# Optimization experiments

Hardware: AMD Instinct MI355X
Metric: run time of the kernel (lower is better)

The kernel has to match this reference:

```python
import jax, jax.numpy as jnp
import numpy as np
from math import sqrt

INPUT, HIDDEN, OUTPUT = 256, 512, 256
B, T = 64, 1024


def setup_inputs() -> dict:
    key = jax.random.key(0)
    k1, k2, k3, k4 = jax.random.split(key, 4)
    x = jax.random.normal(k1, (B, T, INPUT), dtype=jnp.float32)
    W_xh = jax.random.normal(k2, (INPUT, HIDDEN), dtype=jnp.float32) * sqrt(2.0 / (INPUT + HIDDEN))
    W_hh = jax.random.normal(k3, (HIDDEN, HIDDEN), dtype=jnp.float32) * sqrt(1.0 / HIDDEN)
    b_h = jnp.zeros((HIDDEN,), dtype=jnp.float32)
    W_hy = jax.random.normal(k4, (HIDDEN, OUTPUT), dtype=jnp.float32) * sqrt(2.0 / (HIDDEN + OUTPUT))
    b_y = jnp.zeros((OUTPUT,), dtype=jnp.float32)
    return {"x": x, "W_xh": W_xh, "W_hh": W_hh, "b_h": b_h, "W_hy": W_hy, "b_y": b_y}


def reference(x, W_xh, W_hh, b_h, W_hy, b_y):
    # Precompute input projection for all timesteps: [B,T,H_in] @ [H_in,H] -> [B,T,H]
    xh = jnp.einsum('bti,ih->bth', x, W_xh) + b_h
    h0 = jnp.zeros((x.shape[0], W_hh.shape[0]), dtype=x.dtype)

    def step(h, xh_t):
        h_new = jnp.tanh(h @ W_hh + xh_t)  # [B,H]
        return h_new, h_new

    # scan over time: xh transposed to [T,B,H]
    _, hs = jax.lax.scan(step, h0, jnp.swapaxes(xh, 0, 1))
    hs = jnp.swapaxes(hs, 0, 1)  # [B,T,H]
    outputs = jnp.einsum('bth,ho->bto', hs, W_hy) + b_y  # [B,T,O]
    return outputs
```

## Files before the change

### kernel.cpp

```cpp
#include <hip/hip_runtime.h>
#include <hip/hip_bf16.h>
#include <hip/hip_fp16.h>


#define BT 65536
#define HID 512
#define NIN 256
#define NOUT 256
#define TSTEPS 1024
#define NBATCH 64

typedef _Float16 hf2_t __attribute__((ext_vector_type(2)));

__device__ __forceinline__ float fdot2(unsigned w, unsigned h, float acc) {
#if __has_builtin(__builtin_amdgcn_fdot2)
    return __builtin_amdgcn_fdot2(__builtin_bit_cast(hf2_t, w),
                                  __builtin_bit_cast(hf2_t, h), acc, false);
#else
    __half2 wv = __builtin_bit_cast(__half2, w);
    __half2 hv = __builtin_bit_cast(__half2, h);
    float2 wf = __half22float2(wv);
    float2 hf = __half22float2(hv);
    return acc + wf.x * hf.x + wf.y * hf.y;
#endif
}

__device__ __forceinline__ float dot4(uint4 w, uint4 h, float acc) {
    acc = fdot2(w.x, h.x, acc);
    acc = fdot2(w.y, h.y, acc);
    acc = fdot2(w.z, h.z, acc);
    acc = fdot2(w.w, h.w, acc);
    return acc;
}

__device__ __forceinline__ unsigned pack2h(float a, float b) {
    unsigned lo = (unsigned)__half_as_ushort(__float2half_rn(a));
    unsigned hi = (unsigned)__half_as_ushort(__float2half_rn(b));
    return lo | (hi << 16);
}

template <int CTRL>
__device__ __forceinline__ float dpp_add(float x) {
    int y = __builtin_amdgcn_mov_dpp(__float_as_int(x), CTRL, 0xF, 0xF, true);
    return x + __int_as_float(y);
}

__device__ __forceinline__ float fast_tanh(float x) {
    float e = __builtin_amdgcn_exp2f(x * 2.8853900817779268f);
    return 1.0f - 2.0f * __builtin_amdgcn_rcpf(e + 1.0f);
}

__device__ __forceinline__ float4 load4f(const float* p) {
    return *(const float4*)p;
}
__device__ __forceinline__ float4 load4f(const __half* p) {
    ushort4 u = *(const ushort4*)p;
    float4 r;
    r.x = __half2float(__ushort_as_half(u.x));
    r.y = __half2float(__ushort_as_half(u.y));
    r.z = __half2float(__ushort_as_half(u.z));
    r.w = __half2float(__ushort_as_half(u.w));
    return r;
}
__device__ __forceinline__ void store1(float* p, float v) { *p = v; }
__device__ __forceinline__ void store1(__half* p, float v) { *p = __float2half_rn(v); }

__global__ __launch_bounds__(256)
void pack_w_kernel(const float* __restrict__ W,
                   unsigned* __restrict__ reg_blob,
                   unsigned* __restrict__ gcol_blob) {
    int t = blockIdx.x;
    int w = threadIdx.x;
    int q = t >> 2, s = t & 3, k0 = 128 * s;
    if (w < 192) {
        int c = w >> 6, m = w & 63;
        int col = 4 * q + c, k = k0 + 2 * m;
        unsigned val = pack2h(W[(size_t)k * HID + col], W[(size_t)(k + 1) * HID + col]);
        int i = w >> 2, u = w & 3;
        reg_blob[i * 2048 + t * 4 + u] = val;
    } else {
        int m = w - 192;
        int col = 4 * q + 3, k = k0 + 2 * m;
        unsigned val = pack2h(W[(size_t)k * HID + col], W[(size_t)(k + 1) * HID + col]);
        int j = m >> 2, u = m & 3;
        gcol_blob[j * 2048 + t * 4 + u] = val;
    }
}

template <typename AT, typename CT>
__global__ __launch_bounds__(256)
void gemm_bias_kernel(const AT* __restrict__ A, const float* __restrict__ B,
                      const float* __restrict__ bias, CT* __restrict__ C,
                      int M, int N, int K) {
    const int TM = 64, TN = 64, TK = 16;
    __shared__ float As[TK][TM];
    __shared__ float Bs[TK][TN + 4];

    int tid = threadIdx.x;
    int tx = tid & 15;
    int ty = tid >> 4;
    int row0 = blockIdx.x * TM;
    int col0 = blockIdx.y * TN;

    float c[4][4];
#pragma unroll
    for (int i = 0; i < 4; ++i)
#pragma unroll
        for (int j = 0; j < 4; ++j) c[i][j] = 0.f;

    for (int kk = 0; kk < K; kk += TK) {
        {
            int ar = tid >> 2;
            int ac = (tid & 3) * 4;
            float4 av = load4f(A + (size_t)(row0 + ar) * K + kk + ac);
            As[ac + 0][ar] = av.x;
            As[ac + 1][ar] = av.y;
            As[ac + 2][ar] = av.z;
            As[ac + 3][ar] = av.w;
        }
        {
            int br = tid >> 4;
            int bc = (tid & 15) * 4;
            float4 bv = *(const float4*)(B + (size_t)(kk + br) * N + col0 + bc);
            *(float4*)&Bs[br][bc] = bv;
        }
        __syncthreads();
#pragma unroll
        for (int k = 0; k < TK; ++k) {
            float4 a = *(const float4*)&As[k][ty * 4];
            float4 b = *(const float4*)&Bs[k][tx * 4];
            float av[4] = {a.x, a.y, a.z, a.w};
            float bv[4] = {b.x, b.y, b.z, b.w};
#pragma unroll
            for (int i = 0; i < 4; ++i)
#pragma unroll
                for (int j = 0; j < 4; ++j) c[i][j] += av[i] * bv[j];
        }
        __syncthreads();
    }

#pragma unroll
    for (int j = 0; j < 4; ++j) {
        float bb = bias[col0 + tx * 4 + j];
#pragma unroll
        for (int i = 0; i < 4; ++i) {
            int r = row0 + ty * 4 + i;
            int cc = col0 + tx * 4 + j;
            store1(&C[(size_t)r * N + cc], c[i][j] + bb);
        }
    }
}

template <typename AT, typename CT>
__global__ __launch_bounds__(256)
void gemm_bias_f16_kernel(const AT* __restrict__ A, const float* __restrict__ B,
                          const float* __restrict__ bias, CT* __restrict__ C,
                          int M, int N, int K) {
    const int TM = 64, TN = 64, TK = 16;
    __shared__ unsigned Asp[TK / 2][TM];
    __shared__ unsigned Bsp[TK / 2][TN + 4];

    int tid = threadIdx.x;
    int tx = tid & 15;
    int ty = tid >> 4;
    int row0 = blockIdx.x * TM;
    int col0 = blockIdx.y * TN;

    float c[4][4];
#pragma unroll
    for (int i = 0; i < 4; ++i)
#pragma unroll
        for (int j = 0; j < 4; ++j) c[i][j] = 0.f;

    for (int kk = 0; kk < K; kk += TK) {
        {
            int ar = tid >> 2;
            int ac = (tid & 3) * 4;
            float4 av = load4f(A + (size_t)(row0 + ar) * K + kk + ac);
            Asp[(ac >> 1) + 0][ar] = pack2h(av.x, av.y);
            Asp[(ac >> 1) + 1][ar] = pack2h(av.z, av.w);
        }
        {
            int k2 = tid >> 5;
            int bc = (tid & 31) * 2;
            const float* b0 = B + (size_t)(kk + 2 * k2) * N + col0 + bc;
            const float* b1 = b0 + N;
            float2 r0 = *(const float2*)b0;
            float2 r1 = *(const float2*)b1;
            Bsp[k2][bc + 0] = pack2h(r0.x, r1.x);
            Bsp[k2][bc + 1] = pack2h(r0.y, r1.y);
        }
        __syncthreads();
#pragma unroll
        for (int k2 = 0; k2 < TK / 2; ++k2) {
            uint4 ap = *(const uint4*)&Asp[k2][ty * 4];
            uint4 bp = *(const uint4*)&Bsp[k2][tx * 4];
            unsigned av[4] = {ap.x, ap.y, ap.z, ap.w};
            unsigned bv[4] = {bp.x, bp.y, bp.z, bp.w};
#pragma unroll
            for (int i = 0; i < 4; ++i)
#pragma unroll
                for (int j = 0; j < 4; ++j) c[i][j] = fdot2(av[i], bv[j], c[i][j]);
        }
        __syncthreads();
    }

#pragma unroll
    for (int j = 0; j < 4; ++j) {
        float bb = bias[col0 + tx * 4 + j];
#pragma unroll
        for (int i = 0; i < 4; ++i) {
            int r = row0 + ty * 4 + i;
            int cc = col0 + tx * 4 + j;
            store1(&C[(size_t)r * N + cc], c[i][j] + bb);
        }
    }
}

template <int GLN>
__global__ __launch_bounds__(512, 2)
void rnn_scan_single(const __half* __restrict__ xh,
                     const uint4* __restrict__ reg_blob,
                     const uint4* __restrict__ gcol_blob,
                     __half* __restrict__ hs) {
    __shared__ __align__(16) __half hbuf[2][4][136];
    extern __shared__ __align__(16) uint4 gl_[];

    const int t = threadIdx.x;
    const int b = blockIdx.x;
    const int s = t & 3;

    uint4 W[48];
#pragma unroll
    for (int i = 0; i < 48; ++i) W[i] = reg_blob[i * 512 + t];
#pragma unroll
    for (int j = 0; j < GLN; ++j) gl_[j * 512 + t] = gcol_blob[j * 512 + t];

    hbuf[0][t >> 7][t & 127] = __ushort_as_half((unsigned short)0);
    hbuf[1][t >> 7][t & 127] = __ushort_as_half((unsigned short)0);
    __syncthreads();

    const __half* xp = xh + (size_t)b * TSTEPS * HID + t;
    __half* hp = hs + (size_t)b * TSTEPS * HID + t;
    const uint4* gb = gcol_blob + t;

#define GETG(j) (((j) < GLN) ? gl_[(j) * 512 + t] : gb[(size_t)(j) * 512])

    int cur = 0;
    __half prev = __ushort_as_half((unsigned short)0);

    for (int step = 0; step < TSTEPS; ++step) {
        float xv = __half2float(xp[(size_t)step * HID]);
        if (step) hp[(size_t)(step - 1) * HID] = prev;

        const uint4* hv = (const uint4*)&hbuf[cur][s][0];
        float a0 = 0.f, a1 = 0.f, a2 = 0.f, a3 = 0.f;

#pragma unroll
        for (int ch = 0; ch < 4; ++ch) {
            uint4 g0 = GETG(ch * 4 + 0);
            uint4 g1 = GETG(ch * 4 + 1);
            uint4 g2 = GETG(ch * 4 + 2);
            uint4 g3 = GETG(ch * 4 + 3);
            uint4 h0 = hv[ch * 4 + 0];
            uint4 h1 = hv[ch * 4 + 1];
            uint4 h2 = hv[ch * 4 + 2];
            uint4 h3 = hv[ch * 4 + 3];
            a0 = dot4(W[ch * 4 + 0], h0, a0);
            a1 = dot4(W[16 + ch * 4 + 0], h0, a1);
            a2 = dot4(W[32 + ch * 4 + 0], h0, a2);
            a0 = dot4(W[ch * 4 + 1], h1, a0);
            a1 = dot4(W[16 + ch * 4 + 1], h1, a1);
            a2 = dot4(W[32 + ch * 4 + 1], h1, a2);
            a0 = dot4(W[ch * 4 + 2], h2, a0);
            a1 = dot4(W[16 + ch * 4 + 2], h2, a1);
            a2 = dot4(W[32 + ch * 4 + 2], h2, a2);
            a0 = dot4(W[ch * 4 + 3], h3, a0);
            a1 = dot4(W[16 + ch * 4 + 3], h3, a1);
            a2 = dot4(W[32 + ch * 4 + 3], h3, a2);
            a3 = dot4(g0, h0, a3);
            a3 = dot4(g1, h1, a3);
            a3 = dot4(g2, h2, a3);
            a3 = dot4(g3, h3, a3);
        }
#undef GETG

        a0 = dpp_add<0xB1>(a0); a0 = dpp_add<0x4E>(a0);
        a1 = dpp_add<0xB1>(a1); a1 = dpp_add<0x4E>(a1);
        a2 = dpp_add<0xB1>(a2); a2 = dpp_add<0x4E>(a2);
        a3 = dpp_add<0xB1>(a3); a3 = dpp_add<0x4E>(a3);
        float tot = (s == 0) ? a0 : (s == 1) ? a1 : (s == 2) ? a2 : a3;

        float hn = fast_tanh(tot + xv);
        prev = __float2half_rn(hn);
        hbuf[cur ^ 1][t >> 7][t & 127] = prev;
        __syncthreads();
        cur ^= 1;
    }
    hp[(size_t)(TSTEPS - 1) * HID] = prev;
}

extern "C" void kernel_launch(void* const* d_in, const int* in_sizes, int n_in,
                              void* d_out, int out_size, void* d_ws, size_t ws_size,
                              hipStream_t stream) {
    const float* x    = (const float*)d_in[0];
    const float* W_xh = (const float*)d_in[1];
    const float* W_hh = (const float*)d_in[2];
    const float* b_h  = (const float*)d_in[3];
    const float* W_hy = (const float*)d_in[4];
    const float* b_y  = (const float*)d_in[5];
    float* out = (float*)d_out;

    char* ws = (char*)d_ws;
    const size_t off_gcol = 48 * 512 * 16;
    const size_t off_xh   = (size_t)1 << 20;
    const size_t off_hs   = off_xh + (size_t)BT * HID * 2;

    unsigned* reg_blob  = (unsigned*)ws;
    unsigned* gcol_blob = (unsigned*)(ws + off_gcol);
    __half*   xh        = (__half*)(ws + off_xh);
    __half*   hs        = (__half*)(ws + off_hs);

    pack_w_kernel<<<dim3(512), dim3(256), 0, stream>>>(W_hh, reg_blob, gcol_blob);

    gemm_bias_kernel<float, __half>
        <<<dim3(BT / 64, HID / 64), dim3(256), 0, stream>>>(x, W_xh, b_h, xh, BT, HID, NIN);

    const int GL16_BYTES = 16 * 512 * 16;
    hipError_t e = hipFuncSetAttribute(
        reinterpret_cast<const void*>(&rnn_scan_single<16>),
        hipFuncAttributeMaxDynamicSharedMemorySize, GL16_BYTES);
    if (e == hipSuccess) {
        rnn_scan_single<16><<<dim3(NBATCH), dim3(512), GL16_BYTES, stream>>>(
            xh, (const uint4*)reg_blob, (const uint4*)gcol_blob, hs);
    } else {
        (void)hipGetLastError();
        rnn_scan_single<7><<<dim3(NBATCH), dim3(512), 7 * 512 * 16, stream>>>(
            xh, (const uint4*)reg_blob, (const uint4*)gcol_blob, hs);
    }

    gemm_bias_f16_kernel<__half, float>
        <<<dim3(BT / 64, NOUT / 64), dim3(256), 0, stream>>>(hs, W_hy, b_y, out, BT, NOUT, HID);
}
```

Measured before the change: 1.887 ms.

## Restructure RNN scan to 8-way K split with 8 columns per thread group

Measured after the change: 1.869 ms. Within noise of the previous version (-1.0%).

```diff
diff --git a/kernel.cpp b/kernel.cpp
--- a/kernel.cpp
+++ b/kernel.cpp
@@ -44,6 +44,11 @@
     int y = __builtin_amdgcn_mov_dpp(__float_as_int(x), CTRL, 0xF, 0xF, true);
     return x + __int_as_float(y);
 }
+template <int CTRL>
+__device__ __forceinline__ float dpp_get(float x) {
+    int y = __builtin_amdgcn_mov_dpp(__float_as_int(x), CTRL, 0xF, 0xF, true);
+    return __int_as_float(y);
+}
 
 __device__ __forceinline__ float fast_tanh(float x) {
     float e = __builtin_amdgcn_exp2f(x * 2.8853900817779268f);
@@ -71,20 +76,14 @@
                    unsigned* __restrict__ gcol_blob) {
     int t = blockIdx.x;
     int w = threadIdx.x;
-    int q = t >> 2, s = t & 3, k0 = 128 * s;
-    if (w < 192) {
-        int c = w >> 6, m = w & 63;
-        int col = 4 * q + c, k = k0 + 2 * m;
-        unsigned val = pack2h(W[(size_t)k * HID + col], W[(size_t)(k + 1) * HID + col]);
-        int i = w >> 2, u = w & 3;
-        reg_blob[i * 2048 + t * 4 + u] = val;
-    } else {
-        int m = w - 192;
-        int col = 4 * q + 3, k = k0 + 2 * m;
-        unsigned val = pack2h(W[(size_t)k * HID + col], W[(size_t)(k + 1) * HID + col]);
-        int j = m >> 2, u = m & 3;
-        gcol_blob[j * 2048 + t * 4 + u] = val;
-    }
+    int i = w >> 2, u = w & 3;
+    int g = t >> 3, s = t & 7;
+    int c = i >> 3, j = i & 7;
+    int col = 8 * g + c;
+    int k = 64 * s + 8 * j + 2 * u;
+    unsigned val = pack2h(W[(size_t)k * HID + col], W[(size_t)(k + 1) * HID + col]);
+    if (i < 48) reg_blob[(i * 512 + t) * 4 + u] = val;
+    else        gcol_blob[((i - 48) * 512 + t) * 4 + u] = val;
 }
 
 template <typename AT, typename CT>
@@ -219,16 +218,16 @@
 
 template <int GLN>
 __global__ __launch_bounds__(512, 2)
-void rnn_scan_single(const __half* __restrict__ xh,
-                     const uint4* __restrict__ reg_blob,
-                     const uint4* __restrict__ gcol_blob,
-                     __half* __restrict__ hs) {
-    __shared__ __align__(16) __half hbuf[2][4][136];
+void rnn_scan8(const __half* __restrict__ xh,
+               const uint4* __restrict__ reg_blob,
+               const uint4* __restrict__ gcol_blob,
+               __half* __restrict__ hs) {
+    __shared__ __align__(16) uint4 hbuf4[2][72];
     extern __shared__ __align__(16) uint4 gl_[];
 
     const int t = threadIdx.x;
     const int b = blockIdx.x;
-    const int s = t & 3;
+    const int g = t >> 3, s = t & 7;
 
     uint4 W[48];
 #pragma unroll
@@ -236,13 +235,19 @@
 #pragma unroll
     for (int j = 0; j < GLN; ++j) gl_[j * 512 + t] = gcol_blob[j * 512 + t];
 
-    hbuf[0][t >> 7][t & 127] = __ushort_as_half((unsigned short)0);
-    hbuf[1][t >> 7][t & 127] = __ushort_as_half((unsigned short)0);
+    if (t < 72) {
+        hbuf4[0][t] = uint4{0u, 0u, 0u, 0u};
+        hbuf4[1][t] = uint4{0u, 0u, 0u, 0u};
+    }
     __syncthreads();
 
-    const __half* xp = xh + (size_t)b * TSTEPS * HID + t;
-    __half* hp = hs + (size_t)b * TSTEPS * HID + t;
+    const int col = 8 * g + s;
+    const __half* xp = xh + (size_t)b * TSTEPS * HID + col;
+    __half* hp = hs + (size_t)b * TSTEPS * HID + col;
     const uint4* gb = gcol_blob + t;
+
+    const int H = col >> 1;
+    const int wordC = ((H >> 5) * 9 + ((H >> 2) & 7)) * 4 + (H & 3);
 
 #define GETG(j) (((j) < GLN) ? gl_[(j) * 512 + t] : gb[(size_t)(j) * 512])
 
@@ -253,47 +258,62 @@
         float xv = __half2float(xp[(size_t)step * HID]);
         if (step) hp[(size_t)(step - 1) * HID] = prev;
 
-        const uint4* hv = (const uint4*)&hbuf[cur][s][0];
-        float a0 = 0.f, a1 = 0.f, a2 = 0.f, a3 = 0.f;
-
-#pragma unroll
-        for (int ch = 0; ch < 4; ++ch) {
-            uint4 g0 = GETG(ch * 4 + 0);
-            uint4 g1 = GETG(ch * 4 + 1);
-            uint4 g2 = GETG(ch * 4 + 2);
-            uint4 g3 = GETG(ch * 4 + 3);
-            uint4 h0 = hv[ch * 4 + 0];
-            uint4 h1 = hv[ch * 4 + 1];
-            uint4 h2 = hv[ch * 4 + 2];
-            uint4 h3 = hv[ch * 4 + 3];
-            a0 = dot4(W[ch * 4 + 0], h0, a0);
-            a1 = dot4(W[16 + ch * 4 + 0], h0, a1);
-            a2 = dot4(W[32 + ch * 4 + 0], h0, a2);
-            a0 = dot4(W[ch * 4 + 1], h1, a0);
-            a1 = dot4(W[16 + ch * 4 + 1], h1, a1);
-            a2 = dot4(W[32 + ch * 4 + 1], h1, a2);
-            a0 = dot4(W[ch * 4 + 2], h2, a0);
-            a1 = dot4(W[16 + ch * 4 + 2], h2, a1);
-            a2 = dot4(W[32 + ch * 4 + 2], h2, a2);
-            a0 = dot4(W[ch * 4 + 3], h3, a0);
-            a1 = dot4(W[16 + ch * 4 + 3], h3, a1);
-            a2 = dot4(W[32 + ch * 4 + 3], h3, a2);
-            a3 = dot4(g0, h0, a3);
-            a3 = dot4(g1, h1, a3);
-            a3 = dot4(g2, h2, a3);
-            a3 = dot4(g3, h3, a3);
+        const uint4* hv = &hbuf4[cur][s * 9];
+        float acc[8];
+#pragma unroll
+        for (int c = 0; c < 8; ++c) acc[c] = 0.f;
+
+#pragma unroll
+        for (int ch = 0; ch < 2; ++ch) {
+            const int j4 = ch * 4;
+            uint4 h0 = hv[j4 + 0];
+            uint4 h1 = hv[j4 + 1];
+            uint4 h2 = hv[j4 + 2];
+            uint4 h3 = hv[j4 + 3];
+#pragma unroll
+            for (int c = 0; c < 6; ++c) {
+                acc[c] = dot4(W[c * 8 + j4 + 0], h0, acc[c]);
+                acc[c] = dot4(W[c * 8 + j4 + 1], h1, acc[c]);
+                acc[c] = dot4(W[c * 8 + j4 + 2], h2, acc[c]);
+                acc[c] = dot4(W[c * 8 + j4 + 3], h3, acc[c]);
+            }
+            {
+                uint4 g0 = GETG(j4 + 0), g1 = GETG(j4 + 1);
+                uint4 g2 = GETG(j4 + 2), g3 = GETG(j4 + 3);
+                acc[6] = dot4(g0, h0, acc[6]); acc[6] = dot4(g1, h1, acc[6]);
+                acc[6] = dot4(g2, h2, acc[6]); acc[6] = dot4(g3, h3, acc[6]);
+            }
+            {
+                uint4 g0 = GETG(8 + j4 + 0), g1 = GETG(8 + j4 + 1);
+                uint4 g2 = GETG(8 + j4 + 2), g3 = GETG(8 + j4 + 3);
+                acc[7] = dot4(g0, h0, acc[7]); acc[7] = dot4(g1, h1, acc[7]);
+                acc[7] = dot4(g2, h2, acc[7]); acc[7] = dot4(g3, h3, acc[7]);
+            }
         }
 #undef GETG
 
-        a0 = dpp_add<0xB1>(a0); a0 = dpp_add<0x4E>(a0);
-        a1 = dpp_add<0xB1>(a1); a1 = dpp_add<0x4E>(a1);
-        a2 = dpp_add<0xB1>(a2); a2 = dpp_add<0x4E>(a2);
-        a3 = dpp_add<0xB1>(a3); a3 = dpp_add<0x4E>(a3);
-        float tot = (s == 0) ? a0 : (s == 1) ? a1 : (s == 2) ? a2 : a3;
+#pragma unroll
+        for (int c = 0; c < 8; ++c) {
+            acc[c] = dpp_add<0xB1>(acc[c]);
+            acc[c] = dpp_add<0x4E>(acc[c]);
+            acc[c] = dpp_add<0x141>(acc[c]);
+        }
+
+        float tot = acc[0];
+        tot = (s == 1) ? acc[1] : tot;
+        tot = (s == 2) ? acc[2] : tot;
+        tot = (s == 3) ? acc[3] : tot;
+        tot = (s == 4) ? acc[4] : tot;
+        tot = (s == 5) ? acc[5] : tot;
+        tot = (s == 6) ? acc[6] : tot;
+        tot = (s == 7) ? acc[7] : tot;
 
         float hn = fast_tanh(tot + xv);
         prev = __float2half_rn(hn);
-        hbuf[cur ^ 1][t >> 7][t & 127] = prev;
+
+        float hi = dpp_get<0xB1>(hn);
+        unsigned* hwp = (unsigned*)&hbuf4[cur ^ 1][0];
+        if (!(s & 1)) hwp[wordC] = pack2h(hn, hi);
         __syncthreads();
         cur ^= 1;
     }
@@ -328,14 +348,14 @@
 
     const int GL16_BYTES = 16 * 512 * 16;
     hipError_t e = hipFuncSetAttribute(
-        reinterpret_cast<const void*>(&rnn_scan_single<16>),
+        reinterpret_cast<const void*>(&rnn_scan8<16>),
         hipFuncAttributeMaxDynamicSharedMemorySize, GL16_BYTES);
     if (e == hipSuccess) {
-        rnn_scan_single<16><<<dim3(NBATCH), dim3(512), GL16_BYTES, stream>>>(
+        rnn_scan8<16><<<dim3(NBATCH), dim3(512), GL16_BYTES, stream>>>(
             xh, (const uint4*)reg_blob, (const uint4*)gcol_blob, hs);
     } else {
         (void)hipGetLastError();
-        rnn_scan_single<7><<<dim3(NBATCH), dim3(512), 7 * 512 * 16, stream>>>(
+        rnn_scan8<7><<<dim3(NBATCH), dim3(512), 7 * 512 * 16, stream>>>(
             xh, (const uint4*)reg_blob, (const uint4*)gcol_blob, hs);
     }
 
```
